# Optimization experiments

Hardware: AMD Instinct MI355X
Metric: run time of the kernel (lower is better)

## Reference

```python
import jax, jax.numpy as jnp
import numpy as np

N = 50000; E = 1600000; F_IN = 32; HEADS = 8; D = 16; HID = HEADS * D
ED = 16; G = 512; MH = 512; MO = 512; SLOPE = 0.2


def setup_inputs() -> dict:
    key = jax.random.key(0)
    ks = jax.random.split(key, 40)
    inp = {}
    inp["x"] = jax.random.normal(ks[0], (N, F_IN), jnp.float32)
    inp["edge_index"] = jax.random.randint(ks[1], (2, E), 0, N)
    inp["edge_attr"] = jax.random.normal(ks[2], (E, ED), jnp.float32)
    inp["batch"] = jnp.sort(jax.random.randint(ks[3], (N,), 0, G))

    def lin(k, fi, fo):
        return jax.random.normal(k, (fi, fo), jnp.float32) / np.sqrt(fi).astype(np.float32)

    i = 4
    dims = [(F_IN, HID), (HID, HID), (HID, HID)]  # GATv2 layers 0..2
    for l, (fi, fo) in enumerate(dims):
        inp[f"Wl{l}"] = lin(ks[i], fi, fo); i += 1
        inp[f"bl{l}"] = jnp.zeros((fo,), jnp.float32)
        inp[f"Wr{l}"] = lin(ks[i], fi, fo); i += 1
        inp[f"br{l}"] = jnp.zeros((fo,), jnp.float32)
        inp[f"We{l}"] = lin(ks[i], ED, fo); i += 1
        inp[f"att{l}"] = jax.random.normal(ks[i], (HEADS, D), jnp.float32) / np.sqrt(D).astype(np.float32); i += 1
        inp[f"b{l}"] = jnp.zeros((fo,), jnp.float32)
    inp["mW1"] = lin(ks[i], HID, MH); i += 1
    inp["mb1"] = jnp.zeros((MH,), jnp.float32)
    inp["ln_g"] = jnp.ones((MH,), jnp.float32)
    inp["ln_b"] = jnp.zeros((MH,), jnp.float32)
    inp["mW2"] = lin(ks[i], MH, MO); i += 1
    inp["mb2"] = jnp.zeros((MO,), jnp.float32)
    return inp


def _gatv2(h, src, dst, ea, Wl, bl, Wr, br, We, att, b):
    # One GATv2Conv layer (eval mode, add_self_loops already applied).
    n = h.shape[0]
    xl = (h @ Wl + bl).reshape(n, HEADS, D)   # source transform
    xr = (h @ Wr + br).reshape(n, HEADS, D)   # target transform
    ee = (ea @ We).reshape(-1, HEADS, D)      # edge transform (no bias in PyG)
    m = xl[src] + xr[dst] + ee                # [E', H, D]
    m = jnp.where(m > 0, m, SLOPE * m)        # LeakyReLU(0.2)
    s = jnp.einsum('ehd,hd->eh', m, att)      # attention logits
    mx = jax.ops.segment_max(s, dst, num_segments=n)
    ex = jnp.exp(s - mx[dst])
    den = jax.ops.segment_sum(ex, dst, num_segments=n)
    alpha = ex / den[dst]                     # softmax over incoming edges
    out = jax.ops.segment_sum(alpha[:, :, None] * xl[src], dst, num_segments=n)
    return out.reshape(n, HEADS * D) + b


def _forward(x, edge_index, edge_attr, batch,
             Wl0, bl0, Wr0, br0, We0, att0, b0,
             Wl1, bl1, Wr1, br1, We1, att1, b1,
             Wl2, bl2, Wr2, br2, We2, att2, b2,
             mW1, mb1, ln_g, ln_b, mW2, mb2):
    src, dst = edge_index[0], edge_index[1]
    # add_self_loops with fill_value='mean': self-loop edge_attr = mean of incoming edge_attr
    cnt = jax.ops.segment_sum(jnp.ones((E,), jnp.float32), dst, num_segments=N)
    loop_attr = jax.ops.segment_sum(edge_attr, dst, num_segments=N) / jnp.clip(cnt, 1.0)[:, None]
    nodes = jnp.arange(N)
    src_f = jnp.concatenate([src, nodes])
    dst_f = jnp.concatenate([dst, nodes])
    ea = jnp.concatenate([edge_attr, loop_attr], axis=0)

    h = jax.nn.relu(_gatv2(x, src_f, dst_f, ea, Wl0, bl0, Wr0, br0, We0, att0, b0))
    h = jax.nn.relu(_gatv2(h, src_f, dst_f, ea, Wl1, bl1, Wr1, br1, We1, att1, b1))
    h = _gatv2(h, src_f, dst_f, ea, Wl2, bl2, Wr2, br2, We2, att2, b2)

    g = jax.ops.segment_sum(h, batch, num_segments=G)  # sum pooling per graph
    z = jax.nn.relu(g @ mW1 + mb1)
    mu = jnp.mean(z, axis=-1, keepdims=True)
    var = jnp.var(z, axis=-1, keepdims=True)
    z = (z - mu) / jnp.sqrt(var + 1e-5) * ln_g + ln_b
    return z @ mW2 + mb2


def reference(x, edge_index, edge_attr, batch,
              Wl0, bl0, Wr0, br0, We0, att0, b0,
              Wl1, bl1, Wr1, br1, We1, att1, b1,
              Wl2, bl2, Wr2, br2, We2, att2, b2,
              mW1, mb1, ln_g, ln_b, mW2, mb2):
    return _forward(x, edge_index, edge_attr, batch,
                    Wl0, bl0, Wr0, br0, We0, att0, b0,
                    Wl1, bl1, Wr1, br1, We1, att1, b1,
                    Wl2, bl2, Wr2, br2, We2, att2, b2,
                    mW1, mb1, ln_g, ln_b, mW2, mb2)
```

## Files before the change

kernel.cpp:

```cpp
#include <hip/hip_runtime.h>
#include <math.h>

#define NN 50000
#define EE 1600000
#define FIN 32
#define HID_ 128
#define ED_ 16
#define GG 512
#define MH_ 512
#define MO_ 512

typedef float v2f __attribute__((ext_vector_type(2)));

#if __has_builtin(__builtin_amdgcn_exp2f)
#define EXP2(x) __builtin_amdgcn_exp2f(x)
#else
#define EXP2(x) exp2f(x)
#endif

template <int CTRL>
__device__ __forceinline__ float dpp_add(float x) {
  int m = __builtin_amdgcn_update_dpp(0, __float_as_int(x), CTRL, 0xF, 0xF, true);
  return x + __int_as_float(m);
}

__device__ __forceinline__ float bfly8(float p) {
  p = dpp_add<0xB1>(p);
  p = dpp_add<0x4E>(p);
  p = dpp_add<0x141>(p);
  return p;
}


__global__ void hist_kernel(const int4* __restrict__ dst4, int* __restrict__ cnt) {
  int e = blockIdx.x * 256 + threadIdx.x;
  if (e >= EE / 4) return;
  int4 d = dst4[e];
  atomicAdd(&cnt[d.x], 1);
  atomicAdd(&cnt[d.y], 1);
  atomicAdd(&cnt[d.z], 1);
  atomicAdd(&cnt[d.w], 1);
}

__global__ __launch_bounds__(256) void scan1_kernel(const int* __restrict__ in, int n,
                                                    int* __restrict__ out,
                                                    int* __restrict__ bsums) {
  int chunk = blockIdx.x;
  int base = chunk * 1024;
  int t = threadIdx.x;
  int idx = base + t * 4;
  int v0 = (idx + 0 < n) ? in[idx + 0] : 0;
  int v1 = (idx + 1 < n) ? in[idx + 1] : 0;
  int v2 = (idx + 2 < n) ? in[idx + 2] : 0;
  int v3 = (idx + 3 < n) ? in[idx + 3] : 0;
  int ts = v0 + v1 + v2 + v3;
  int lane = t & 63, w = t >> 6;
  int s = ts;
#pragma unroll
  for (int off = 1; off < 64; off <<= 1) {
    int o = __shfl_up(s, off);
    if (lane >= off) s += o;
  }
  __shared__ int wsum[4];
  if (lane == 63) wsum[w] = s;
  __syncthreads();
  int woff = 0;
  for (int i = 0; i < w; i++) woff += wsum[i];
  int excl = woff + s - ts;
  int run = excl;
  run += v0; if (idx + 0 < n) out[idx + 0] = run;
  run += v1; if (idx + 1 < n) out[idx + 1] = run;
  run += v2; if (idx + 2 < n) out[idx + 2] = run;
  run += v3; if (idx + 3 < n) out[idx + 3] = run;
  if (t == 255) bsums[chunk] = woff + s;
}

__global__ void scan_add_kernel(int* __restrict__ rowptr, const int* __restrict__ bscan, int n) {
  int i = blockIdx.x * 256 + threadIdx.x;
  if (i == 0) rowptr[0] = 0;
  if (i < n) {
    int chunk = i >> 10;
    if (chunk > 0) rowptr[1 + i] += bscan[chunk - 1];
  }
}

__global__ void scatter_kernel(const int4* __restrict__ src4, const int4* __restrict__ dst4,
                               const int* __restrict__ rowptr, int* __restrict__ fill,
                               int2* __restrict__ csr) {
  int e = blockIdx.x * 256 + threadIdx.x;
  if (e >= EE / 4) return;
  int4 s = src4[e];
  int4 d = dst4[e];
  int eb = e * 4;
  int p0 = rowptr[d.x] + atomicAdd(&fill[d.x], 1);
  csr[p0] = make_int2(s.x, eb + 0);
  int p1 = rowptr[d.y] + atomicAdd(&fill[d.y], 1);
  csr[p1] = make_int2(s.y, eb + 1);
  int p2 = rowptr[d.z] + atomicAdd(&fill[d.z], 1);
  csr[p2] = make_int2(s.z, eb + 2);
  int p3 = rowptr[d.w] + atomicAdd(&fill[d.w], 1);
  csr[p3] = make_int2(s.w, eb + 3);
}


template <int F>
__global__ __launch_bounds__(256) void node_transform(const float* __restrict__ h,
                                                      const float* __restrict__ Wlm,
                                                      const float* __restrict__ blm,
                                                      const float* __restrict__ Wrm,
                                                      const float* __restrict__ brm,
                                                      float* __restrict__ xl,
                                                      float* __restrict__ xr, int nnodes) {
  __shared__ float hs[F * 32];
  int v0 = blockIdx.x * 32;
  int t = threadIdx.x;
  for (int idx = t; idx < 32 * F; idx += 256) {
    int i = idx / F, k = idx - i * F;
    hs[k * 32 + i] = (v0 + i < nnodes) ? h[(size_t)(v0 + i) * F + k] : 0.f;
  }
  __syncthreads();
  bool isL = t < 128;
  int q = t & 63;
  int nh = (t >> 6) & 1;
  const float* Wm = isL ? Wlm : Wrm;
  v2f acc[16];
#pragma unroll
  for (int i = 0; i < 16; i++) acc[i] = (v2f){0.f, 0.f};
  for (int k = 0; k < F; k++) {
    v2f w = *(const v2f*)(Wm + k * 128 + 2 * q);
    const float4* hk4 = (const float4*)(hs + k * 32 + nh * 16);
#pragma unroll
    for (int r = 0; r < 4; r++) {
      float4 hv = hk4[r];
      acc[4 * r + 0] = __builtin_elementwise_fma((v2f){hv.x, hv.x}, w, acc[4 * r + 0]);
      acc[4 * r + 1] = __builtin_elementwise_fma((v2f){hv.y, hv.y}, w, acc[4 * r + 1]);
      acc[4 * r + 2] = __builtin_elementwise_fma((v2f){hv.z, hv.z}, w, acc[4 * r + 2]);
      acc[4 * r + 3] = __builtin_elementwise_fma((v2f){hv.w, hv.w}, w, acc[4 * r + 3]);
    }
  }
  const float* bm = isL ? blm : brm;
  v2f b = *(const v2f*)(bm + 2 * q);
  float* dstp = isL ? xl : xr;
  int base = v0 + nh * 16;
#pragma unroll
  for (int i = 0; i < 16; i++) {
    if (base + i < nnodes)
      *(v2f*)(dstp + (size_t)(base + i) * 128 + 2 * q) = acc[i] + b;
  }
}


template <int LAYER0>
__global__ __launch_bounds__(256, 4) void gat_aggregate(
    const float* __restrict__ xl, const float* __restrict__ xr,
    const int* __restrict__ rowptr, const int2* __restrict__ csr,
    const float* __restrict__ ea, float* __restrict__ la,
    const float* __restrict__ We, const float* __restrict__ att,
    const float* __restrict__ bias, float* __restrict__ hout, int relu) {
  int wid = threadIdx.x >> 6, lane = threadIdx.x & 63;
  int v = __builtin_amdgcn_readfirstlane(blockIdx.x * 4 + wid);
  if (v >= NN) return;
  int c = 2 * lane;
  v2f wec[16];
#pragma unroll
  for (int k = 0; k < 16; k++) wec[k] = *(const v2f*)(We + k * 128 + c);
#pragma unroll
  for (int k = 0; k < 16; k++) {
    float tx = wec[k].x, ty = wec[k].y;
    asm volatile("" : "+v"(tx), "+v"(ty));
    wec[k] = (v2f){tx, ty};
  }
  const float L2E = 1.44269504088896340736f;
  v2f av = *(const v2f*)(att + c) * L2E;
  v2f xrv = *(const v2f*)(xr + (size_t)v * 128 + c);
  {
    float t0 = av.x, t1 = av.y, t2 = xrv.x, t3 = xrv.y;
    asm volatile("" : "+v"(t0), "+v"(t1), "+v"(t2), "+v"(t3));
    av = (v2f){t0, t1};
    xrv = (v2f){t2, t3};
  }

  auto score = [&](int u, const float* eaP, v2f& xu) -> float {
    xu = *(const v2f*)(xl + (size_t)u * 128 + c);
    v2f m = xrv + xu;
#pragma unroll
    for (int k = 0; k < 16; k++) {
      float e = eaP[k];
      m = __builtin_elementwise_fma((v2f){e, e}, wec[k], m);
    }
    m = __builtin_elementwise_max(m, 0.2f * m);
    v2f qq = av * m;
    return bfly8(qq.x + qq.y);
  };

  int d16 = lane & 15;
  v2f acc = (v2f){0.f, 0.f};
  float den = 0.f;
  float la_f = 0.f;
  int start = __builtin_amdgcn_readfirstlane(rowptr[v]);
  int end = __builtin_amdgcn_readfirstlane(rowptr[v + 1]);
  int j = start;
  for (; j + 4 <= end; j += 4) {
    int2 e0 = csr[j], e1 = csr[j + 1], e2 = csr[j + 2], e3 = csr[j + 3];
    int u0 = __builtin_amdgcn_readfirstlane(e0.x);
    int u1 = __builtin_amdgcn_readfirstlane(e1.x);
    int u2 = __builtin_amdgcn_readfirstlane(e2.x);
    int u3 = __builtin_amdgcn_readfirstlane(e3.x);
    const float* p0 = ea + (size_t)__builtin_amdgcn_readfirstlane(e0.y) * 16;
    const float* p1 = ea + (size_t)__builtin_amdgcn_readfirstlane(e1.y) * 16;
    const float* p2 = ea + (size_t)__builtin_amdgcn_readfirstlane(e2.y) * 16;
    const float* p3 = ea + (size_t)__builtin_amdgcn_readfirstlane(e3.y) * 16;
    if (LAYER0) la_f += (p0[d16] + p1[d16]) + (p2[d16] + p3[d16]);
    v2f x0, x1, x2, x3;
    float s0 = score(u0, p0, x0);
    float s1 = score(u1, p1, x1);
    float s2 = score(u2, p2, x2);
    float s3 = score(u3, p3, x3);
    float w0 = EXP2(s0), w1 = EXP2(s1), w2 = EXP2(s2), w3 = EXP2(s3);
    den += (w0 + w1) + (w2 + w3);
    acc = __builtin_elementwise_fma((v2f){w0, w0}, x0,
          __builtin_elementwise_fma((v2f){w1, w1}, x1,
          __builtin_elementwise_fma((v2f){w2, w2}, x2,
          __builtin_elementwise_fma((v2f){w3, w3}, x3, acc))));
  }
  for (; j < end; ++j) {
    int2 e0 = csr[j];
    int u = __builtin_amdgcn_readfirstlane(e0.x);
    const float* p0 = ea + (size_t)__builtin_amdgcn_readfirstlane(e0.y) * 16;
    if (LAYER0) la_f += p0[d16];
    v2f xu;
    float p = score(u, p0, xu);
    float w = EXP2(p);
    den += w;
    acc = __builtin_elementwise_fma((v2f){w, w}, xu, acc);
  }

  int deg = end - start;
  if (LAYER0) {
    float invdeg = (deg > 0) ? 1.f / (float)deg : 0.f;
    la_f *= invdeg;
    if (lane < 16) la[(size_t)v * 16 + d16] = la_f;
    v2f xu = *(const v2f*)(xl + (size_t)v * 128 + c);
    v2f m = xrv + xu;
#pragma unroll
    for (int k = 0; k < 16; k++) {
      float e = __int_as_float(__builtin_amdgcn_readlane(__float_as_int(la_f), k));
      m = __builtin_elementwise_fma((v2f){e, e}, wec[k], m);
    }
    m = __builtin_elementwise_max(m, 0.2f * m);
    v2f qq = av * m;
    float p = bfly8(qq.x + qq.y);
    float w = EXP2(p);
    den += w;
    acc = __builtin_elementwise_fma((v2f){w, w}, xu, acc);
  } else {
    v2f xu;
    float p = score(v, la + (size_t)v * 16, xu);
    float w = EXP2(p);
    den += w;
    acc = __builtin_elementwise_fma((v2f){w, w}, xu, acc);
  }

  float invd = 1.f / den;
  v2f bv = *(const v2f*)(bias + c);
  v2f o = __builtin_elementwise_fma(acc, (v2f){invd, invd}, bv);
  if (relu) o = __builtin_elementwise_max(o, (v2f){0.f, 0.f});
  *(v2f*)(hout + (size_t)v * 128 + c) = o;
}


__global__ void gptr_kernel(const int* __restrict__ batch, int* __restrict__ gptr) {
  int g = blockIdx.x * 256 + threadIdx.x;
  if (g > GG) return;
  int lo = 0, hi = NN;
  while (lo < hi) {
    int mid = (lo + hi) >> 1;
    if (batch[mid] < g) lo = mid + 1; else hi = mid;
  }
  gptr[g] = lo;
}

__global__ void pool_kernel(const float* __restrict__ h, const int* __restrict__ gptr,
                            float* __restrict__ gp) {
  int gi = blockIdx.x;
  int c = threadIdx.x;
  int s = gptr[gi], e = gptr[gi + 1];
  float acc = 0.f;
  for (int v = s; v < e; v++) acc += h[(size_t)v * 128 + c];
  gp[gi * 128 + c] = acc;
}

__global__ __launch_bounds__(256) void mlp1_kernel(const float* __restrict__ gp,
                                                   const float* __restrict__ mW1,
                                                   const float* __restrict__ mb1,
                                                   const float* __restrict__ lng,
                                                   const float* __restrict__ lnb,
                                                   float* __restrict__ z) {
  int row = blockIdx.x;
  int t = threadIdx.x;
  __shared__ float gs[128];
  if (t < 128) gs[t] = gp[row * 128 + t];
  __syncthreads();
  int c0 = t, c1 = t + 256;
  float z0 = 0.f, z1 = 0.f;
  for (int k = 0; k < 128; k++) {
    float gk = gs[k];
    z0 = fmaf(gk, mW1[k * 512 + c0], z0);
    z1 = fmaf(gk, mW1[k * 512 + c1], z1);
  }
  z0 += mb1[c0]; z1 += mb1[c1];
  z0 = fmaxf(z0, 0.f); z1 = fmaxf(z1, 0.f);
  float s = z0 + z1, q = z0 * z0 + z1 * z1;
#pragma unroll
  for (int off = 32; off > 0; off >>= 1) {
    s += __shfl_xor(s, off);
    q += __shfl_xor(q, off);
  }
  __shared__ float red[8];
  int lane = t & 63, w = t >> 6;
  if (lane == 0) { red[w] = s; red[4 + w] = q; }
  __syncthreads();
  float S = red[0] + red[1] + red[2] + red[3];
  float Q = red[4] + red[5] + red[6] + red[7];
  float mu = S / 512.f;
  float var = Q / 512.f - mu * mu;
  float inv = 1.f / sqrtf(var + 1e-5f);
  z[row * 512 + c0] = (z0 - mu) * inv * lng[c0] + lnb[c0];
  z[row * 512 + c1] = (z1 - mu) * inv * lng[c1] + lnb[c1];
}

__global__ __launch_bounds__(256) void mlp2_kernel(const float* __restrict__ z,
                                                   const float* __restrict__ mW2,
                                                   const float* __restrict__ mb2,
                                                   float* __restrict__ out) {
  int row = blockIdx.x;
  int t = threadIdx.x;
  __shared__ float zs[512];
  for (int i = t; i < 512; i += 256) zs[i] = z[row * 512 + i];
  __syncthreads();
  int c0 = t, c1 = t + 256;
  float o0 = 0.f, o1 = 0.f;
  for (int k = 0; k < 512; k++) {
    float zk = zs[k];
    o0 = fmaf(zk, mW2[k * 512 + c0], o0);
    o1 = fmaf(zk, mW2[k * 512 + c1], o1);
  }
  out[row * 512 + c0] = o0 + mb2[c0];
  out[row * 512 + c1] = o1 + mb2[c1];
}


extern "C" void kernel_launch(void* const* d_in, const int* in_sizes, int n_in,
                              void* d_out, int out_size, void* d_ws, size_t ws_size,
                              hipStream_t stream) {
  const float* x = (const float*)d_in[0];
  const int* ei = (const int*)d_in[1];
  const int* srcE = ei;
  const int* dstE = ei + EE;
  const float* ea = (const float*)d_in[2];
  const int* batch = (const int*)d_in[3];
  const float* Wl[3] = {(const float*)d_in[4], (const float*)d_in[11], (const float*)d_in[18]};
  const float* bl[3] = {(const float*)d_in[5], (const float*)d_in[12], (const float*)d_in[19]};
  const float* Wr[3] = {(const float*)d_in[6], (const float*)d_in[13], (const float*)d_in[20]};
  const float* br[3] = {(const float*)d_in[7], (const float*)d_in[14], (const float*)d_in[21]};
  const float* Wek[3] = {(const float*)d_in[8], (const float*)d_in[15], (const float*)d_in[22]};
  const float* attk[3] = {(const float*)d_in[9], (const float*)d_in[16], (const float*)d_in[23]};
  const float* bk[3] = {(const float*)d_in[10], (const float*)d_in[17], (const float*)d_in[24]};
  const float* mW1 = (const float*)d_in[25];
  const float* mb1 = (const float*)d_in[26];
  const float* lng = (const float*)d_in[27];
  const float* lnb = (const float*)d_in[28];
  const float* mW2 = (const float*)d_in[29];
  const float* mb2 = (const float*)d_in[30];
  float* outp = (float*)d_out;

  char* W = (char*)d_ws;
  size_t off = 0;
  auto take = [&](size_t b) -> void* {
    void* p = W + off;
    off += (b + 255) & ~(size_t)255;
    return p;
  };
  int* cnt = (int*)take(NN * 4);
  int* rowptr = (int*)take((NN + 1) * 4);
  int* bsums = (int*)take(64 * 4);
  int* bscan = (int*)take(64 * 4);
  int* dummy = (int*)take(64 * 4);
  int2* csr = (int2*)take((size_t)EE * 8);
  float* la = (float*)take((size_t)NN * 16 * 4);
  float* xl = (float*)take((size_t)NN * HID_ * 4);
  float* xr = (float*)take((size_t)NN * HID_ * 4);
  float* hbuf = (float*)take((size_t)NN * HID_ * 4);
  int* gptr = (int*)take((GG + 1) * 4);
  float* gpool = (float*)take((size_t)GG * HID_ * 4);
  float* z = (float*)take((size_t)GG * MH_ * 4);
  (void)ws_size; (void)n_in; (void)in_sizes; (void)out_size;

  hipMemsetAsync(cnt, 0, NN * 4, stream);
  hist_kernel<<<(EE / 4 + 255) / 256, 256, 0, stream>>>((const int4*)dstE, cnt);
  scan1_kernel<<<49, 256, 0, stream>>>(cnt, NN, rowptr + 1, bsums);
  scan1_kernel<<<1, 256, 0, stream>>>(bsums, 49, bscan, dummy);
  scan_add_kernel<<<(NN + 255) / 256, 256, 0, stream>>>(rowptr, bscan, NN);
  hipMemsetAsync(cnt, 0, NN * 4, stream);
  scatter_kernel<<<(EE / 4 + 255) / 256, 256, 0, stream>>>((const int4*)srcE, (const int4*)dstE,
                                                           rowptr, cnt, csr);

  for (int l = 0; l < 3; l++) {
    if (l == 0)
      node_transform<FIN><<<(NN + 31) / 32, 256, 0, stream>>>(x, Wl[0], bl[0], Wr[0], br[0],
                                                              xl, xr, NN);
    else
      node_transform<HID_><<<(NN + 31) / 32, 256, 0, stream>>>(hbuf, Wl[l], bl[l], Wr[l], br[l],
                                                               xl, xr, NN);
    if (l == 0)
      gat_aggregate<1><<<(NN + 3) / 4, 256, 0, stream>>>(xl, xr, rowptr, csr, ea, la,
                                                         Wek[0], attk[0], bk[0], hbuf, 1);
    else
      gat_aggregate<0><<<(NN + 3) / 4, 256, 0, stream>>>(xl, xr, rowptr, csr, ea, la,
                                                         Wek[l], attk[l], bk[l], hbuf,
                                                         (l < 2) ? 1 : 0);
  }

  gptr_kernel<<<3, 256, 0, stream>>>(batch, gptr);
  pool_kernel<<<GG, 128, 0, stream>>>(hbuf, gptr, gpool);
  mlp1_kernel<<<GG, 256, 0, stream>>>(gpool, mW1, mb1, lng, lnb, z);
  mlp2_kernel<<<GG, 256, 0, stream>>>(z, mW2, mb2, outp);
}
```

Baseline: 1.027 ms.

## Reload edge weights per edge in aggregation, pad node-transform LDS tile

The aggregation kernel no longer keeps the 16 We columns pinned in VGPRs. It reloads them from global/L1 inside the unrolled 4-edge loop, interleaving the four edge FMAs per weight load, and drops the launch-bounds min-blocks hint. The xl gathers for the four edges are issued up front to expose memory-level parallelism. Separately, the node_transform shared tile gets a stride of 34 instead of 32 with v2f reads, to cut LDS bank conflicts. The tradeoff is more load instructions per edge in exchange for lower register pressure, and the occupancy hint is removed.

Result: faster. 1.001 ms (-2.5%).

```diff
diff --git a/kernel.cpp b/kernel.cpp
--- a/kernel.cpp
+++ b/kernel.cpp
@@ -111,12 +111,12 @@
                                                       const float* __restrict__ brm,
                                                       float* __restrict__ xl,
                                                       float* __restrict__ xr, int nnodes) {
-  __shared__ float hs[F * 32];
+  __shared__ float hs[F * 34];
   int v0 = blockIdx.x * 32;
   int t = threadIdx.x;
   for (int idx = t; idx < 32 * F; idx += 256) {
     int i = idx / F, k = idx - i * F;
-    hs[k * 32 + i] = (v0 + i < nnodes) ? h[(size_t)(v0 + i) * F + k] : 0.f;
+    hs[k * 34 + i] = (v0 + i < nnodes) ? h[(size_t)(v0 + i) * F + k] : 0.f;
   }
   __syncthreads();
   bool isL = t < 128;
@@ -128,14 +128,12 @@
   for (int i = 0; i < 16; i++) acc[i] = (v2f){0.f, 0.f};
   for (int k = 0; k < F; k++) {
     v2f w = *(const v2f*)(Wm + k * 128 + 2 * q);
-    const float4* hk4 = (const float4*)(hs + k * 32 + nh * 16);
-#pragma unroll
-    for (int r = 0; r < 4; r++) {
-      float4 hv = hk4[r];
-      acc[4 * r + 0] = __builtin_elementwise_fma((v2f){hv.x, hv.x}, w, acc[4 * r + 0]);
-      acc[4 * r + 1] = __builtin_elementwise_fma((v2f){hv.y, hv.y}, w, acc[4 * r + 1]);
-      acc[4 * r + 2] = __builtin_elementwise_fma((v2f){hv.z, hv.z}, w, acc[4 * r + 2]);
-      acc[4 * r + 3] = __builtin_elementwise_fma((v2f){hv.w, hv.w}, w, acc[4 * r + 3]);
+    const v2f* hk2 = (const v2f*)(hs + k * 34 + nh * 16);
+#pragma unroll
+    for (int r = 0; r < 8; r++) {
+      v2f hv = hk2[r];
+      acc[2 * r + 0] = __builtin_elementwise_fma((v2f){hv.x, hv.x}, w, acc[2 * r + 0]);
+      acc[2 * r + 1] = __builtin_elementwise_fma((v2f){hv.y, hv.y}, w, acc[2 * r + 1]);
     }
   }
   const float* bm = isL ? blm : brm;
@@ -151,7 +149,7 @@
 
 
 template <int LAYER0>
-__global__ __launch_bounds__(256, 4) void gat_aggregate(
+__global__ __launch_bounds__(256) void gat_aggregate(
     const float* __restrict__ xl, const float* __restrict__ xr,
     const int* __restrict__ rowptr, const int2* __restrict__ csr,
     const float* __restrict__ ea, float* __restrict__ la,
@@ -161,32 +159,17 @@
   int v = __builtin_amdgcn_readfirstlane(blockIdx.x * 4 + wid);
   if (v >= NN) return;
   int c = 2 * lane;
-  v2f wec[16];
-#pragma unroll
-  for (int k = 0; k < 16; k++) wec[k] = *(const v2f*)(We + k * 128 + c);
-#pragma unroll
-  for (int k = 0; k < 16; k++) {
-    float tx = wec[k].x, ty = wec[k].y;
-    asm volatile("" : "+v"(tx), "+v"(ty));
-    wec[k] = (v2f){tx, ty};
-  }
+  const float* Wc = We + c;
   const float L2E = 1.44269504088896340736f;
   v2f av = *(const v2f*)(att + c) * L2E;
   v2f xrv = *(const v2f*)(xr + (size_t)v * 128 + c);
-  {
-    float t0 = av.x, t1 = av.y, t2 = xrv.x, t3 = xrv.y;
-    asm volatile("" : "+v"(t0), "+v"(t1), "+v"(t2), "+v"(t3));
-    av = (v2f){t0, t1};
-    xrv = (v2f){t2, t3};
-  }
-
-  auto score = [&](int u, const float* eaP, v2f& xu) -> float {
-    xu = *(const v2f*)(xl + (size_t)u * 128 + c);
+
+  auto score = [&](const float* eaP, v2f xu) -> float {
     v2f m = xrv + xu;
 #pragma unroll
     for (int k = 0; k < 16; k++) {
       float e = eaP[k];
-      m = __builtin_elementwise_fma((v2f){e, e}, wec[k], m);
+      m = __builtin_elementwise_fma((v2f){e, e}, *(const v2f*)(Wc + k * 128), m);
     }
     m = __builtin_elementwise_max(m, 0.2f * m);
     v2f qq = av * m;
@@ -211,11 +194,28 @@
     const float* p2 = ea + (size_t)__builtin_amdgcn_readfirstlane(e2.y) * 16;
     const float* p3 = ea + (size_t)__builtin_amdgcn_readfirstlane(e3.y) * 16;
     if (LAYER0) la_f += (p0[d16] + p1[d16]) + (p2[d16] + p3[d16]);
-    v2f x0, x1, x2, x3;
-    float s0 = score(u0, p0, x0);
-    float s1 = score(u1, p1, x1);
-    float s2 = score(u2, p2, x2);
-    float s3 = score(u3, p3, x3);
+    v2f x0 = *(const v2f*)(xl + (size_t)u0 * 128 + c);
+    v2f x1 = *(const v2f*)(xl + (size_t)u1 * 128 + c);
+    v2f x2 = *(const v2f*)(xl + (size_t)u2 * 128 + c);
+    v2f x3 = *(const v2f*)(xl + (size_t)u3 * 128 + c);
+    v2f m0 = xrv + x0, m1 = xrv + x1, m2 = xrv + x2, m3 = xrv + x3;
+#pragma unroll
+    for (int k = 0; k < 16; k++) {
+      v2f w = *(const v2f*)(Wc + k * 128);
+      m0 = __builtin_elementwise_fma((v2f){p0[k], p0[k]}, w, m0);
+      m1 = __builtin_elementwise_fma((v2f){p1[k], p1[k]}, w, m1);
+      m2 = __builtin_elementwise_fma((v2f){p2[k], p2[k]}, w, m2);
+      m3 = __builtin_elementwise_fma((v2f){p3[k], p3[k]}, w, m3);
+    }
+    m0 = __builtin_elementwise_max(m0, 0.2f * m0);
+    m1 = __builtin_elementwise_max(m1, 0.2f * m1);
+    m2 = __builtin_elementwise_max(m2, 0.2f * m2);
+    m3 = __builtin_elementwise_max(m3, 0.2f * m3);
+    v2f q0 = av * m0, q1 = av * m1, q2 = av * m2, q3 = av * m3;
+    float s0 = bfly8(q0.x + q0.y);
+    float s1 = bfly8(q1.x + q1.y);
+    float s2 = bfly8(q2.x + q2.y);
+    float s3 = bfly8(q3.x + q3.y);
     float w0 = EXP2(s0), w1 = EXP2(s1), w2 = EXP2(s2), w3 = EXP2(s3);
     den += (w0 + w1) + (w2 + w3);
     acc = __builtin_elementwise_fma((v2f){w0, w0}, x0,
@@ -228,37 +228,36 @@
     int u = __builtin_amdgcn_readfirstlane(e0.x);
     const float* p0 = ea + (size_t)__builtin_amdgcn_readfirstlane(e0.y) * 16;
     if (LAYER0) la_f += p0[d16];
-    v2f xu;
-    float p = score(u, p0, xu);
+    v2f xu = *(const v2f*)(xl + (size_t)u * 128 + c);
+    float p = score(p0, xu);
     float w = EXP2(p);
     den += w;
     acc = __builtin_elementwise_fma((v2f){w, w}, xu, acc);
   }
 
   int deg = end - start;
+  v2f xuv = *(const v2f*)(xl + (size_t)v * 128 + c);
   if (LAYER0) {
     float invdeg = (deg > 0) ? 1.f / (float)deg : 0.f;
     la_f *= invdeg;
     if (lane < 16) la[(size_t)v * 16 + d16] = la_f;
-    v2f xu = *(const v2f*)(xl + (size_t)v * 128 + c);
-    v2f m = xrv + xu;
+    v2f m = xrv + xuv;
 #pragma unroll
     for (int k = 0; k < 16; k++) {
       float e = __int_as_float(__builtin_amdgcn_readlane(__float_as_int(la_f), k));
-      m = __builtin_elementwise_fma((v2f){e, e}, wec[k], m);
+      m = __builtin_elementwise_fma((v2f){e, e}, *(const v2f*)(Wc + k * 128), m);
     }
     m = __builtin_elementwise_max(m, 0.2f * m);
     v2f qq = av * m;
     float p = bfly8(qq.x + qq.y);
     float w = EXP2(p);
     den += w;
-    acc = __builtin_elementwise_fma((v2f){w, w}, xu, acc);
+    acc = __builtin_elementwise_fma((v2f){w, w}, xuv, acc);
   } else {
-    v2f xu;
-    float p = score(v, la + (size_t)v * 16, xu);
+    float p = score(la + (size_t)v * 16, xuv);
     float w = EXP2(p);
     den += w;
-    acc = __builtin_elementwise_fma((v2f){w, w}, xu, acc);
+    acc = __builtin_elementwise_fma((v2f){w, w}, xuv, acc);
   }
 
   float invd = 1.f / den;
```

## Store xl/xr node features in fp16 to halve gather traffic in aggregation

Applied to the files above, without the earlier changes.

Node transform outputs xl and xr are now written as half2 instead of float, and the aggregate kernel gathers them as half2 and converts them to float. This halves the bytes per random neighbor gather, which dominates the edge loop. The change also pads the shared tile stride to 34, drops the occupancy hint and the asm register pins, and moves the self-loop score ahead of the edge loop for non-first layers. The cost is reduced precision of the transformed features, which could affect accuracy tolerance.

Measured after the change: 882.1 us, median of 2. 1.16x faster.

```diff
diff --git a/kernel.cpp b/kernel.cpp
--- a/kernel.cpp
+++ b/kernel.cpp
@@ -1,4 +1,5 @@
 #include <hip/hip_runtime.h>
+#include <hip/hip_fp16.h>
 #include <math.h>
 
 #define NN 50000
@@ -29,6 +30,11 @@
   p = dpp_add<0x4E>(p);
   p = dpp_add<0x141>(p);
   return p;
+}
+
+__device__ __forceinline__ v2f h2f(__half2 h) {
+  float2 f = __half22float2(h);
+  return (v2f){f.x, f.y};
 }
 
 
@@ -109,14 +115,14 @@
                                                       const float* __restrict__ blm,
                                                       const float* __restrict__ Wrm,
                                                       const float* __restrict__ brm,
-                                                      float* __restrict__ xl,
-                                                      float* __restrict__ xr, int nnodes) {
-  __shared__ float hs[F * 32];
+                                                      __half2* __restrict__ xl,
+                                                      __half2* __restrict__ xr, int nnodes) {
+  __shared__ float hs[F * 34];
   int v0 = blockIdx.x * 32;
   int t = threadIdx.x;
   for (int idx = t; idx < 32 * F; idx += 256) {
     int i = idx / F, k = idx - i * F;
-    hs[k * 32 + i] = (v0 + i < nnodes) ? h[(size_t)(v0 + i) * F + k] : 0.f;
+    hs[k * 34 + i] = (v0 + i < nnodes) ? h[(size_t)(v0 + i) * F + k] : 0.f;
   }
   __syncthreads();
   bool isL = t < 128;
@@ -128,31 +134,31 @@
   for (int i = 0; i < 16; i++) acc[i] = (v2f){0.f, 0.f};
   for (int k = 0; k < F; k++) {
     v2f w = *(const v2f*)(Wm + k * 128 + 2 * q);
-    const float4* hk4 = (const float4*)(hs + k * 32 + nh * 16);
-#pragma unroll
-    for (int r = 0; r < 4; r++) {
-      float4 hv = hk4[r];
-      acc[4 * r + 0] = __builtin_elementwise_fma((v2f){hv.x, hv.x}, w, acc[4 * r + 0]);
-      acc[4 * r + 1] = __builtin_elementwise_fma((v2f){hv.y, hv.y}, w, acc[4 * r + 1]);
-      acc[4 * r + 2] = __builtin_elementwise_fma((v2f){hv.z, hv.z}, w, acc[4 * r + 2]);
-      acc[4 * r + 3] = __builtin_elementwise_fma((v2f){hv.w, hv.w}, w, acc[4 * r + 3]);
+    const v2f* hk2 = (const v2f*)(hs + k * 34 + nh * 16);
+#pragma unroll
+    for (int r = 0; r < 8; r++) {
+      v2f hv = hk2[r];
+      acc[2 * r + 0] = __builtin_elementwise_fma((v2f){hv.x, hv.x}, w, acc[2 * r + 0]);
+      acc[2 * r + 1] = __builtin_elementwise_fma((v2f){hv.y, hv.y}, w, acc[2 * r + 1]);
     }
   }
   const float* bm = isL ? blm : brm;
   v2f b = *(const v2f*)(bm + 2 * q);
-  float* dstp = isL ? xl : xr;
+  __half2* dstp = isL ? xl : xr;
   int base = v0 + nh * 16;
 #pragma unroll
   for (int i = 0; i < 16; i++) {
-    if (base + i < nnodes)
-      *(v2f*)(dstp + (size_t)(base + i) * 128 + 2 * q) = acc[i] + b;
+    if (base + i < nnodes) {
+      v2f o = acc[i] + b;
+      dstp[(size_t)(base + i) * 64 + q] = __floats2half2_rn(o.x, o.y);
+    }
   }
 }
 
 
 template <int LAYER0>
-__global__ __launch_bounds__(256, 4) void gat_aggregate(
-    const float* __restrict__ xl, const float* __restrict__ xr,
+__global__ __launch_bounds__(256) void gat_aggregate(
+    const __half2* __restrict__ xl, const __half2* __restrict__ xr,
     const int* __restrict__ rowptr, const int2* __restrict__ csr,
     const float* __restrict__ ea, float* __restrict__ la,
     const float* __restrict__ We, const float* __restrict__ att,
@@ -164,24 +170,12 @@
   v2f wec[16];
 #pragma unroll
   for (int k = 0; k < 16; k++) wec[k] = *(const v2f*)(We + k * 128 + c);
-#pragma unroll
-  for (int k = 0; k < 16; k++) {
-    float tx = wec[k].x, ty = wec[k].y;
-    asm volatile("" : "+v"(tx), "+v"(ty));
-    wec[k] = (v2f){tx, ty};
-  }
   const float L2E = 1.44269504088896340736f;
   v2f av = *(const v2f*)(att + c) * L2E;
-  v2f xrv = *(const v2f*)(xr + (size_t)v * 128 + c);
-  {
-    float t0 = av.x, t1 = av.y, t2 = xrv.x, t3 = xrv.y;
-    asm volatile("" : "+v"(t0), "+v"(t1), "+v"(t2), "+v"(t3));
-    av = (v2f){t0, t1};
-    xrv = (v2f){t2, t3};
-  }
+  v2f xrv = h2f(xr[(size_t)v * 64 + lane]);
 
   auto score = [&](int u, const float* eaP, v2f& xu) -> float {
-    xu = *(const v2f*)(xl + (size_t)u * 128 + c);
+    xu = h2f(xl[(size_t)u * 64 + lane]);
     v2f m = xrv + xu;
 #pragma unroll
     for (int k = 0; k < 16; k++) {
@@ -197,6 +191,13 @@
   v2f acc = (v2f){0.f, 0.f};
   float den = 0.f;
   float la_f = 0.f;
+  if (!LAYER0) {
+    v2f xu;
+    float p = score(v, la + (size_t)v * 16, xu);
+    float w = EXP2(p);
+    den = w;
+    acc = (v2f){w, w} * xu;
+  }
   int start = __builtin_amdgcn_readfirstlane(rowptr[v]);
   int end = __builtin_amdgcn_readfirstlane(rowptr[v + 1]);
   int j = start;
@@ -234,13 +235,12 @@
     den += w;
     acc = __builtin_elementwise_fma((v2f){w, w}, xu, acc);
   }
-
-  int deg = end - start;
   if (LAYER0) {
+    int deg = end - start;
     float invdeg = (deg > 0) ? 1.f / (float)deg : 0.f;
     la_f *= invdeg;
     if (lane < 16) la[(size_t)v * 16 + d16] = la_f;
-    v2f xu = *(const v2f*)(xl + (size_t)v * 128 + c);
+    v2f xu = h2f(xl[(size_t)v * 64 + lane]);
     v2f m = xrv + xu;
 #pragma unroll
     for (int k = 0; k < 16; k++) {
@@ -253,14 +253,7 @@
     float w = EXP2(p);
     den += w;
     acc = __builtin_elementwise_fma((v2f){w, w}, xu, acc);
-  } else {
-    v2f xu;
-    float p = score(v, la + (size_t)v * 16, xu);
-    float w = EXP2(p);
-    den += w;
-    acc = __builtin_elementwise_fma((v2f){w, w}, xu, acc);
-  }
-
+  }
   float invd = 1.f / den;
   v2f bv = *(const v2f*)(bias + c);
   v2f o = __builtin_elementwise_fma(acc, (v2f){invd, invd}, bv);
@@ -388,8 +381,8 @@
   int* dummy = (int*)take(64 * 4);
   int2* csr = (int2*)take((size_t)EE * 8);
   float* la = (float*)take((size_t)NN * 16 * 4);
-  float* xl = (float*)take((size_t)NN * HID_ * 4);
-  float* xr = (float*)take((size_t)NN * HID_ * 4);
+  __half2* xl = (__half2*)take((size_t)NN * 64 * 4);
+  __half2* xr = (__half2*)take((size_t)NN * 64 * 4);
   float* hbuf = (float*)take((size_t)NN * HID_ * 4);
   int* gptr = (int*)take((GG + 1) * 4);
   float* gpool = (float*)take((size_t)GG * HID_ * 4);
```
